# Kernel optimization log

Measured on AMD Instinct MI355X. Metric: run time of the kernel, lower is better.

Reference implementation:

```python
import jax, jax.numpy as jnp
import numpy as np

V = [8192, 2048, 512, 128, 32]   # vertex counts per mesh level
S = 9                            # spiral length
T = 64                           # number of audio frames
OC = [32, 64, 64, 128]           # out_channels
LAT = 64                         # latent_channels


def _spiral_conv(x, idx, w, b):
    # x: [B, Vi, C], idx: [Vi, S] -> gather spiral neighborhoods, flatten, linear
    B = x.shape[0]
    n, s = idx.shape
    g = x[:, idx.reshape(-1), :].reshape(B, n, -1)  # [B, Vi, S*C]
    return g @ w + b


def _pool(x, row, col, val, out_size):
    # sparse COO matmul along vertex dim: out[b, r, :] += val * x[b, c, :]
    g = x[:, col, :] * val[None, :, None]
    return jnp.zeros((x.shape[0], out_size, x.shape[2]), x.dtype).at[:, row, :].add(g)


def setup_inputs():
    key = jax.random.key(0)
    keys = iter(jax.random.split(key, 80))
    def nrm(shape, scale=0.05):
        return jax.random.normal(next(keys), shape, jnp.float32) * scale
    inp = {}
    inp["hidden_states"] = jax.random.normal(next(keys), (1, T, 768), jnp.float32)
    inp["actor"] = jax.random.normal(next(keys), (1, V[0], 3), jnp.float32)
    inp["audio_w"] = nrm((768, LAT)); inp["audio_b"] = jnp.zeros((LAT,), jnp.float32)
    enc_dims = [(3 * S, OC[0]), (OC[0] * S, OC[1]), (OC[1] * S, OC[2]), (OC[2] * S, OC[3])]
    for i, (a, b) in enumerate(enc_dims):
        inp[f"enc{i}_w"] = nrm((a, b)); inp[f"enc{i}_b"] = jnp.zeros((b,), jnp.float32)
    inp["enc_lat_w"] = nrm((V[4] * OC[3], LAT)); inp["enc_lat_b"] = jnp.zeros((LAT,), jnp.float32)
    inp["dec_lin_w"] = nrm((2 * LAT, V[4] * OC[3])); inp["dec_lin_b"] = jnp.zeros((V[4] * OC[3],), jnp.float32)
    dec_dims = [(OC[3] * S, OC[3]), (OC[3] * S, OC[2]), (OC[2] * S, OC[1]), (OC[1] * S, OC[0])]
    for i, (a, b) in enumerate(dec_dims):
        inp[f"dec{i}_w"] = nrm((a, b)); inp[f"dec{i}_b"] = jnp.zeros((b,), jnp.float32)
    inp["dec_out_w"] = nrm((OC[0] * S, 3)); inp["dec_out_b"] = jnp.zeros((3,), jnp.float32)
    for i in range(4):
        inp[f"spiral{i}"] = jax.random.randint(next(keys), (V[i], S), 0, V[i])
    for i in range(4):
        vin, vout = V[i], V[i + 1]
        inp[f"down{i}_row"] = jnp.repeat(jnp.arange(vout), 3)
        inp[f"down{i}_col"] = jax.random.randint(next(keys), (3 * vout,), 0, vin)
        inp[f"down{i}_val"] = jax.random.uniform(next(keys), (3 * vout,), jnp.float32) / 3.0
        inp[f"up{i}_row"] = jnp.repeat(jnp.arange(vin), 3)
        inp[f"up{i}_col"] = jax.random.randint(next(keys), (3 * vin,), 0, vout)
        inp[f"up{i}_val"] = jax.random.uniform(next(keys), (3 * vin,), jnp.float32) / 3.0
    return inp


def reference(hidden_states, actor, audio_w, audio_b,
              enc0_w, enc0_b, enc1_w, enc1_b, enc2_w, enc2_b, enc3_w, enc3_b,
              enc_lat_w, enc_lat_b,
              dec_lin_w, dec_lin_b, dec0_w, dec0_b, dec1_w, dec1_b,
              dec2_w, dec2_b, dec3_w, dec3_b, dec_out_w, dec_out_b,
              spiral0, spiral1, spiral2, spiral3,
              down0_row, down0_col, down0_val, down1_row, down1_col, down1_val,
              down2_row, down2_col, down2_val, down3_row, down3_col, down3_val,
              up0_row, up0_col, up0_val, up1_row, up1_col, up1_val,
              up2_row, up2_col, up2_val, up3_row, up3_col, up3_val):
    spirals = [spiral0, spiral1, spiral2, spiral3]
    enc_p = [(enc0_w, enc0_b), (enc1_w, enc1_b), (enc2_w, enc2_b), (enc3_w, enc3_b)]
    dec_p = [(dec0_w, dec0_b), (dec1_w, dec1_b), (dec2_w, dec2_b), (dec3_w, dec3_b)]
    down = [(down0_row, down0_col, down0_val), (down1_row, down1_col, down1_val),
            (down2_row, down2_col, down2_val), (down3_row, down3_col, down3_val)]
    up = [(up0_row, up0_col, up0_val), (up1_row, up1_col, up1_val),
          (up2_row, up2_col, up2_val), (up3_row, up3_col, up3_val)]

    # ---- encode(actor): conv -> elu -> pool per level, then flatten linear ----
    x = actor  # [1, V0, 3]
    for i in range(4):
        w, b = enc_p[i]
        x = jax.nn.elu(_spiral_conv(x, spirals[i], w, b))
        r, c, v = down[i]
        x = _pool(x, r, c, v, V[i + 1])
    actor_emb = x.reshape(1, -1) @ enc_lat_w + enc_lat_b  # [1, LAT]

    # ---- audio embedding and latent concat ----
    audio_emb = hidden_states[0] @ audio_w + audio_b       # [T, LAT]
    latent = jnp.concatenate(
        [audio_emb, jnp.broadcast_to(actor_emb, audio_emb.shape)], axis=-1)  # [T, 2*LAT]

    # ---- decode all frames at once (original loops per frame; batched over T) ----
    x = (latent @ dec_lin_w + dec_lin_b).reshape(-1, V[4], OC[3])  # [T, V4, OC3]
    for i in range(4):
        lvl = 3 - i
        r, c, v = up[lvl]
        x = _pool(x, r, c, v, V[lvl])
        w, b = dec_p[i]
        x = jax.nn.elu(_spiral_conv(x, spirals[lvl], w, b))
    x = _spiral_conv(x, spirals[0], dec_out_w, dec_out_b)  # [T, V0, 3]
    return x + actor  # broadcast actor (displacement prediction), pred_sequence[1:]
```

## Files before the change

### kernel.cpp

```cpp
#include <hip/hip_runtime.h>
#include <hip/hip_bf16.h>

typedef __hip_bfloat16 bf16;
typedef __attribute__((ext_vector_type(8))) short short8v;
typedef __attribute__((ext_vector_type(16))) float f32x16;

__device__ __forceinline__ float tof(float v){ return v; }
__device__ __forceinline__ float tof(bf16 v){ return __bfloat162float(v); }
__device__ __forceinline__ void sto(float* p, float v){ *p = v; }
__device__ __forceinline__ void sto(bf16* p, float v){ *p = __float2bfloat16(v); }
__device__ __forceinline__ short f2bs(float f){ bf16 h = __float2bfloat16(f); return *(short*)&h; }
__device__ __forceinline__ float bsu2f(short s){
    return __uint_as_float(((unsigned)(unsigned short)s) << 16);
}

__device__ __forceinline__ void sto4(float* p, float4 v){ *(float4*)p = v; }
__device__ __forceinline__ void sto4(bf16* p, float4 v){
    short4 s; s.x=f2bs(v.x); s.y=f2bs(v.y); s.z=f2bs(v.z); s.w=f2bs(v.w);
    *(short4*)p = s;
}

__device__ __forceinline__ void swz_t(int b, int bs, int& t, int& rem){
    int x = b & 7, k = b >> 3;
    t = x*8 + (k >> bs);
    rem = k & ((1 << bs) - 1);
}

__global__ __launch_bounds__(256) void k_prep(
    const float* __restrict__ w0, const float* __restrict__ w1,
    const float* __restrict__ w2, const float* __restrict__ w3,
    const float* __restrict__ w4,
    short* __restrict__ wt0, short* __restrict__ wt1,
    short* __restrict__ wt2, short* __restrict__ wt3,
    short* __restrict__ wt4,
    const float* __restrict__ hs, const float* __restrict__ aw,
    const float* __restrict__ ab, float* __restrict__ aemb)
{
    __shared__ float red[4][64];
    int b = blockIdx.x, tid = threadIdx.x;
    if (b < 1080){
        const float* w; short* wt; int K, nsh, i;
        if      (b < 576) { w = w0; wt = wt0; K = 1152; nsh = 7; i = b*256 + tid; }
        else if (b < 864) { w = w1; wt = wt1; K = 1152; nsh = 6; i = (b-576)*256 + tid; }
        else if (b < 1008){ w = w2; wt = wt2; K = 576;  nsh = 6; i = (b-864)*256 + tid; }
        else              { w = w3; wt = wt3; K = 576;  nsh = 5; i = (b-1008)*256 + tid; }
        int k = i >> nsh, n = i & ((1 << nsh) - 1);
        wt[n*K + k] = f2bs(w[i]);
    } else if (b < 1116){
        int i = (b - 1080)*256 + tid;
        int k = i >> 5, n = i & 31;
        wt4[n*288 + k] = (n < 3) ? f2bs(w4[k*3 + n]) : (short)0;
    } else {
        int t = b - 1116;
        int kg = tid >> 6, l = tid & 63;
        const float* h = hs + t*768;
        float acc = 0.f;
        int k0 = kg*192;
        #pragma unroll 8
        for (int k = k0; k < k0 + 192; k++) acc += h[k] * aw[k*64 + l];
        red[kg][l] = acc;
        __syncthreads();
        if (kg == 0)
            aemb[t*64 + l] = red[0][l] + red[1][l] + red[2][l] + red[3][l] + ab[l];
    }
}

__global__ __launch_bounds__(256) void k_enclat(const float* __restrict__ flat,
    const float* __restrict__ w, const float* __restrict__ b, float* __restrict__ out)
{
    __shared__ float red[256];
    int l = blockIdx.x, tid = threadIdx.x;
    float acc = 0.f;
    for (int k = tid; k < 4096; k += 256) acc += flat[k] * w[k*64 + l];
    red[tid] = acc; __syncthreads();
    for (int s = 128; s > 0; s >>= 1){ if (tid < s) red[tid] += red[tid+s]; __syncthreads(); }
    if (tid == 0) out[l] = red[0] + b[l];
}

__global__ __launch_bounds__(256) void k_declin4(const float* __restrict__ ae,
    const float* __restrict__ pe, const float* __restrict__ w, const float* __restrict__ b,
    bf16* __restrict__ out)
{
    int n4 = blockIdx.x*256 + threadIdx.x;
    int t = blockIdx.y;
    float4 acc = *(const float4*)&b[n4*4];
    const float* a = ae + t*64;
    #pragma unroll 4
    for (int k = 0; k < 64; k++){
        float av = a[k];
        float4 wv = *(const float4*)&w[(size_t)k*4096 + n4*4];
        acc.x += av*wv.x; acc.y += av*wv.y; acc.z += av*wv.z; acc.w += av*wv.w;
    }
    #pragma unroll 4
    for (int k = 0; k < 64; k++){
        float pv = pe[k];
        float4 wv = *(const float4*)&w[(size_t)(64+k)*4096 + n4*4];
        acc.x += pv*wv.x; acc.y += pv*wv.y; acc.z += pv*wv.z; acc.w += pv*wv.w;
    }
    sto4(&out[(size_t)t*4096 + n4*4], acc);
}

__global__ __launch_bounds__(256) void k_pool4(const float* __restrict__ xin,
    const int* __restrict__ col, const float* __restrict__ val, float* __restrict__ out,
    int total4, int c4mask, int cs, int vomask, int vos, int Vi)
{
    int i = blockIdx.x*256 + threadIdx.x;
    if (i >= total4) return;
    int c4 = i & c4mask;
    int rv = i >> cs;
    int r  = rv & vomask;
    int t  = rv >> vos;
    int C  = (c4mask + 1) << 2;
    const float* xt = xin + (size_t)t * Vi * C;
    int r3 = 3*r;
    int j0 = col[r3], j1 = col[r3+1], j2 = col[r3+2];
    float v0 = val[r3], v1 = val[r3+1], v2 = val[r3+2];
    int c = c4 << 2;
    float4 a = *(const float4*)&xt[(size_t)j0*C + c];
    float4 b = *(const float4*)&xt[(size_t)j1*C + c];
    float4 d = *(const float4*)&xt[(size_t)j2*C + c];
    float4 o;
    o.x = v0*a.x + v1*b.x + v2*d.x;
    o.y = v0*a.y + v1*b.y + v2*d.y;
    o.z = v0*a.z + v1*b.z + v2*d.z;
    o.w = v0*a.w + v1*b.w + v2*d.w;
    sto4(&out[(size_t)i << 2], o);
}

__global__ __launch_bounds__(256) void k_poolb(const bf16* __restrict__ xin,
    const int* __restrict__ col, const float* __restrict__ val, bf16* __restrict__ out,
    int c8mask, int cs, int vom, int vshin, int cshift, int bs, int ept8)
{
    int t, rem; swz_t(blockIdx.x, bs, t, rem);
    int il = rem*256 + threadIdx.x;
    int c8 = il & c8mask;
    int r  = (il >> cs) & vom;
    size_t i = (size_t)t * ept8 + il;
    const bf16* xt = xin + ((size_t)t << (vshin + cshift));
    int r3 = 3*r;
    int j0 = col[r3], j1 = col[r3+1], j2 = col[r3+2];
    float v0 = val[r3], v1 = val[r3+1], v2 = val[r3+2];
    int c = c8 << 3;
    short8v a = *(const short8v*)&xt[((size_t)j0 << cshift) + c];
    short8v b = *(const short8v*)&xt[((size_t)j1 << cshift) + c];
    short8v d = *(const short8v*)&xt[((size_t)j2 << cshift) + c];
    short8v o;
    #pragma unroll
    for (int q = 0; q < 8; q++)
        o[q] = f2bs(v0*bsu2f(a[q]) + v1*bsu2f(b[q]) + v2*bsu2f(d[q]));
    *(short8v*)&out[i << 3] = o;
}

template<int KTOT, int CSHIFT, int NTOT, typename TOUT>
__global__ __launch_bounds__(256) void k_conv_p3(
    const bf16* __restrict__ xin, const int* __restrict__ spiral,
    const short* __restrict__ wt, const float* __restrict__ bias, TOUT* __restrict__ out,
    int vshift, int bs, int nbshift)
{
    constexpr int NCH  = KTOT >> 6;
    constexpr int CSUB = CSHIFT - 6;
    __shared__ short lds_a[2*128*72];
    __shared__ short lds_b[2*32*72];
    const int tid = threadIdx.x;
    const int lane = tid & 63;
    const int wv = tid >> 6;
    const int col = lane & 31;
    const int half = lane >> 5;

    int t, rem; swz_t(blockIdx.x, bs, t, rem);
    const int nb = rem & ((1 << nbshift) - 1);
    const int vt = rem >> nbshift;
    const int mbase = vt*128;
    const size_t xslab = (size_t)t << (vshift + CSHIFT);

    const int am = tid >> 3;
    const int ak = (tid & 7) << 3;
    const int bn = tid >> 3;
    const int bk = (tid & 7) << 3;

    short8v pa[3][4];
    short8v pb[3];

    auto issue = [&](int ch, int st){
        int s = ch >> CSUB;
        int coff = ((ch & ((1 << CSUB) - 1)) << 6) + ak;
        #pragma unroll
        for (int u = 0; u < 4; u++){
            int j = spiral[(mbase + am + u*32)*9 + s];
            pa[st][u] = *(const short8v*)&xin[xslab + ((size_t)j << CSHIFT) + coff];
        }
        pb[st] = *(const short8v*)&wt[(size_t)(nb*32 + bn)*KTOT + (ch << 6) + bk];
    };
    auto commit = [&](int ch, int st){
        short* la = lds_a + (ch & 1)*(128*72);
        short* lb = lds_b + (ch & 1)*(32*72);
        #pragma unroll
        for (int u = 0; u < 4; u++)
            *(short8v*)&la[(am + u*32)*72 + ak] = pa[st][u];
        *(short8v*)&lb[bn*72 + bk] = pb[st];
    };

    f32x16 acc;
    {
        float bv = bias[nb*32 + col];
        #pragma unroll
        for (int r = 0; r < 16; r++) acc[r] = bv;
    }

    issue(0, 0);
    issue(1, 1);
    issue(2, 2);
    commit(0, 0);
    __syncthreads();
    #pragma unroll
    for (int ch = 0; ch < NCH; ch++){
        if (ch + 3 < NCH) issue(ch + 3, ch % 3);
        const short* la = lds_a + (ch & 1)*(128*72);
        const short* lb = lds_b + (ch & 1)*(32*72);
        #pragma unroll
        for (int ks = 0; ks < 4; ks++){
            short8v b = *(const short8v*)&lb[col*72 + ks*16 + half*8];
            short8v a = *(const short8v*)&la[(wv*32 + col)*72 + ks*16 + half*8];
            acc = __builtin_amdgcn_mfma_f32_32x32x16_bf16(a, b, acc, 0, 0, 0);
        }
        if (ch + 1 < NCH) commit(ch + 1, (ch + 1) % 3);
        __syncthreads();
    }
    size_t mb = ((size_t)t << vshift) + mbase + wv*32;
    #pragma unroll
    for (int r = 0; r < 16; r++){
        int row = (r & 3) + 8*(r >> 2) + 4*half;
        float vv = acc[r];
        vv = vv > 0.f ? vv : __expf(vv) - 1.f;
        sto(&out[(mb + row)*NTOT + nb*32 + col], vv);
    }
}

__global__ __launch_bounds__(256) void k_outmfma(
    const bf16* __restrict__ xin, const int* __restrict__ spiral,
    const short* __restrict__ wt, const float* __restrict__ bias,
    const float* __restrict__ actor, float* __restrict__ out)
{
    __shared__ short lds_a[256*36];
    __shared__ short lds_b[32*36];
    const int tid = threadIdx.x;
    const int lane = tid & 63;
    const int wv = tid >> 6;
    const int col = lane & 31;
    const int half = lane >> 5;

    int t, rem; swz_t(blockIdx.x, 5, t, rem);
    const int mbase = rem*256;
    const size_t xslab = (size_t)t << 18;

    short8v pa[4];
    short8v pb;
    const int am = tid >> 2;
    const int ak = (tid & 3) << 3;

    auto issue = [&](int s){
        #pragma unroll
        for (int u = 0; u < 4; u++){
            int j = spiral[(mbase + am + u*64)*9 + s];
            pa[u] = *(const short8v*)&xin[xslab + ((size_t)j << 5) + ak];
        }
        if (tid < 128)
            pb = *(const short8v*)&wt[am*288 + s*32 + ak];
    };
    auto commit = [&](){
        #pragma unroll
        for (int u = 0; u < 4; u++)
            *(short8v*)&lds_a[(am + u*64)*36 + ak] = pa[u];
        if (tid < 128)
            *(short8v*)&lds_b[am*36 + ak] = pb;
    };

    f32x16 acc[2];
    {
        float bv = (col < 3) ? bias[col] : 0.f;
        #pragma unroll
        for (int h = 0; h < 2; h++)
            #pragma unroll
            for (int r = 0; r < 16; r++) acc[h][r] = bv;
    }

    issue(0); commit(); __syncthreads();
    #pragma unroll
    for (int s = 0; s < 9; s++){
        if (s + 1 < 9) issue(s + 1);
        #pragma unroll
        for (int ks = 0; ks < 2; ks++){
            short8v b = *(short8v*)&lds_b[col*36 + ks*16 + half*8];
            #pragma unroll
            for (int h = 0; h < 2; h++){
                short8v a = *(short8v*)&lds_a[(h*128 + wv*32 + col)*36 + ks*16 + half*8];
                acc[h] = __builtin_amdgcn_mfma_f32_32x32x16_bf16(a, b, acc[h], 0, 0, 0);
            }
        }
        __syncthreads();
        if (s + 1 < 9){ commit(); __syncthreads(); }
    }
    if (col < 3){
        #pragma unroll
        for (int h = 0; h < 2; h++){
            int rowb = mbase + h*128 + wv*32;
            #pragma unroll
            for (int r = 0; r < 16; r++){
                int row = rowb + (r & 3) + 8*(r >> 2) + 4*half;
                out[(((size_t)t << 13) + row)*3 + col] = acc[h][r] + actor[row*3 + col];
            }
        }
    }
}

template<typename TIN>
__global__ __launch_bounds__(256) void k_conv(const TIN* __restrict__ xin,
    const int* __restrict__ spiral, const float* __restrict__ w, const float* __restrict__ bias,
    float* __restrict__ out, int TV, int V, int vshift, int C, int O2, int o2shift,
    int K, int KP, int MT)
{
    extern __shared__ float lds[];
    const int S = 9;
    int tid = threadIdx.x;
    int O = O2 << 1;
    int gmbase = blockIdx.x * MT;

    int total = MT * K;
    for (int e = tid; e < total; e += 256){
        int m = e / K, k = e - m*K;
        int gm = gmbase + m;
        if (gm < TV){
            int t = gm >> vshift, v = gm & (V-1);
            int s = k / C, c = k - s*C;
            int jj = spiral[v*S + s];
            lds[m*KP + k] = tof(xin[((size_t)t*V + jj)*C + c]);
        }
    }
    __syncthreads();

    int m = tid >> o2shift;
    int o = tid & (O2 - 1);
    int gm = gmbase + m;
    if (gm >= TV) return;
    const float* g  = lds + m*KP;
    const float* wp = w + 2*o;
    float acc0 = bias[2*o];
    float acc1 = bias[2*o+1];
    int K4 = K & ~3;
    for (int k = 0; k < K4; k += 4){
        float4 g4 = *(const float4*)(g + k);
        float2 w0 = *(const float2*)(wp + (size_t)k    *O);
        float2 w1 = *(const float2*)(wp + (size_t)(k+1)*O);
        float2 w2 = *(const float2*)(wp + (size_t)(k+2)*O);
        float2 w3 = *(const float2*)(wp + (size_t)(k+3)*O);
        acc0 += g4.x*w0.x + g4.y*w1.x + g4.z*w2.x + g4.w*w3.x;
        acc1 += g4.x*w0.y + g4.y*w1.y + g4.z*w2.y + g4.w*w3.y;
    }
    for (int k = K4; k < K; k++){
        float gv = g[k];
        acc0 += gv * wp[(size_t)k*O];
        acc1 += gv * wp[(size_t)k*O + 1];
    }
    acc0 = acc0 > 0.f ? acc0 : __expf(acc0) - 1.f;
    acc1 = acc1 > 0.f ? acc1 : __expf(acc1) - 1.f;
    float2 r; r.x = acc0; r.y = acc1;
    *(float2*)(out + (size_t)gm*O + 2*o) = r;
}

extern "C" void kernel_launch(void* const* d_in, const int* in_sizes, int n_in,
                              void* d_out, int out_size, void* d_ws, size_t ws_size,
                              hipStream_t stream)
{
    (void)n_in; (void)out_size; (void)ws_size;
    const float* hs        = (const float*)d_in[0];
    const float* actor     = (const float*)d_in[1];
    const float* audio_w   = (const float*)d_in[2];
    const float* audio_b   = (const float*)d_in[3];
    const float* enc_w[4]  = {(const float*)d_in[4],(const float*)d_in[6],(const float*)d_in[8],(const float*)d_in[10]};
    const float* enc_b[4]  = {(const float*)d_in[5],(const float*)d_in[7],(const float*)d_in[9],(const float*)d_in[11]};
    const float* enc_lat_w = (const float*)d_in[12];
    const float* enc_lat_b = (const float*)d_in[13];
    const float* dec_lin_w = (const float*)d_in[14];
    const float* dec_lin_b = (const float*)d_in[15];
    const float* dec_w[4]  = {(const float*)d_in[16],(const float*)d_in[18],(const float*)d_in[20],(const float*)d_in[22]};
    const float* dec_b[4]  = {(const float*)d_in[17],(const float*)d_in[19],(const float*)d_in[21],(const float*)d_in[23]};
    const float* dec_out_w = (const float*)d_in[24];
    const float* dec_out_b = (const float*)d_in[25];
    const int*   spiral[4] = {(const int*)d_in[26],(const int*)d_in[27],(const int*)d_in[28],(const int*)d_in[29]};

    const int* dcol[4]; const float* dval[4]; const int* ucol[4]; const float* uval[4];
    bool interleaved = (in_sizes[33] == 3*8192);
    for (int i = 0; i < 4; i++){
        if (interleaved){
            int b = 30 + 6*i;
            dcol[i] = (const int*)d_in[b+1]; dval[i] = (const float*)d_in[b+2];
            ucol[i] = (const int*)d_in[b+4]; uval[i] = (const float*)d_in[b+5];
        } else {
            dcol[i] = (const int*)d_in[31+3*i]; dval[i] = (const float*)d_in[32+3*i];
            ucol[i] = (const int*)d_in[43+3*i]; uval[i] = (const float*)d_in[44+3*i];
        }
    }

    char* ws = (char*)d_ws;
    size_t off = 0;
    auto alloc = [&](size_t bytes)->char* {
        char* p = ws + off; off += (bytes + 255) & ~(size_t)255; return p;
    };
    float* encX0 = (float*)alloc((size_t)262144*4);
    float* encP0 = (float*)alloc((size_t)65536*4);
    float* encX1 = (float*)alloc((size_t)131072*4);
    float* encP1 = (float*)alloc((size_t)32768*4);
    float* encX2 = (float*)alloc((size_t)32768*4);
    float* encP2 = (float*)alloc((size_t)8192*4);
    float* encX3 = (float*)alloc((size_t)16384*4);
    float* encP3 = (float*)alloc((size_t)4096*4);
    float* aemb  = (float*)alloc((size_t)4096*4);
    float* pemb  = (float*)alloc((size_t)64*4);
    short* wt0   = (short*)alloc((size_t)147456*2);
    short* wt1   = (short*)alloc((size_t)73728*2);
    short* wt2   = (short*)alloc((size_t)36864*2);
    short* wt3   = (short*)alloc((size_t)18432*2);
    short* wt4   = (short*)alloc((size_t)9216*2);
    bf16*  Pb    = (bf16*)alloc((size_t)36*1048576);
    bf16*  Qb    = (bf16*)alloc((size_t)68*1048576);

    k_prep<<<1180,256,0,stream>>>(dec_w[0], dec_w[1], dec_w[2], dec_w[3], dec_out_w,
                                  wt0, wt1, wt2, wt3, wt4, hs, audio_w, audio_b, aemb);

    k_conv<float><<<512,256, 16*28*4, stream>>>(actor, spiral[0], enc_w[0], enc_b[0], encX0, 8192, 8192,13,   3,16,4,  27,  28,16);
    k_pool4<<<64,256,0,stream>>>(encX0, dcol[0], dval[0], encP0, 16384, 7,3, 2047,11, 8192);
    k_conv<float><<<256,256, 8*292*4, stream>>>(encP0, spiral[1], enc_w[1], enc_b[1], encX1, 2048, 2048,11,  32,32,5, 288, 292, 8);
    k_pool4<<<32,256,0,stream>>>(encX1, dcol[1], dval[1], encP1, 8192, 15,4, 511,9, 2048);
    k_conv<float><<<64,256, 8*580*4, stream>>>(encP1, spiral[2], enc_w[2], enc_b[2], encX2, 512, 512,9,  64,32,5, 576, 580, 8);
    k_pool4<<<8,256,0,stream>>>(encX2, dcol[2], dval[2], encP2, 2048, 15,4, 127,7, 512);
    k_conv<float><<<32,256, 4*580*4, stream>>>(encP2, spiral[3], enc_w[3], enc_b[3], encX3, 128, 128,7,  64,64,6, 576, 580, 4);
    k_pool4<<<4,256,0,stream>>>(encX3, dcol[3], dval[3], encP3, 1024, 31,5, 31,5, 128);
    k_enclat<<<64,256,0,stream>>>(encP3, enc_lat_w, enc_lat_b, pemb);

    k_declin4<<<dim3(4,64),256,0,stream>>>(aemb, pemb, dec_lin_w, dec_lin_b, Pb);

    k_poolb<<<512,256,0,stream>>>(Pb, ucol[3], uval[3], Qb, 15,4, 127, 5,7, 3, 2048);
    k_conv_p3<1152,7,128,bf16><<<256,256,0,stream>>>(Qb, spiral[3], wt0, dec_b[0], Pb, 7, 2, 2);

    k_poolb<<<2048,256,0,stream>>>(Pb, ucol[2], uval[2], Qb, 15,4, 511, 7,7, 5, 8192);
    k_conv_p3<1152,7,64,bf16><<<512,256,0,stream>>>(Qb, spiral[2], wt1, dec_b[1], Pb, 9, 3, 1);

    k_poolb<<<4096,256,0,stream>>>(Pb, ucol[1], uval[1], Qb, 7,3, 2047, 9,6, 6, 16384);
    k_conv_p3<576,6,64,bf16><<<2048,256,0,stream>>>(Qb, spiral[1], wt2, dec_b[2], Pb, 11, 5, 1);

    k_poolb<<<16384,256,0,stream>>>(Pb, ucol[0], uval[0], Qb, 7,3, 8191, 11,6, 8, 65536);
    k_conv_p3<576,6,32,bf16><<<4096,256,0,stream>>>(Qb, spiral[0], wt3, dec_b[3], Pb, 13, 6, 0);

    k_outmfma<<<2048,256,0,stream>>>(Pb, spiral[0], wt4, dec_out_b, actor, (float*)d_out);
}
```

Baseline: 436.4 us.

## Load spiral-gathered A fragments directly into MFMA registers in output conv

The final output spiral conv no longer stages gathered neighbour rows through LDS with per-step barriers. Each lane now loads its A fragment straight from global memory using spiral indices held in registers. The whole weight matrix is preloaded into LDS once, and each block covers 128 rows instead of 256, which doubles the grid. This drops the barrier-heavy staging loop, but the 16-byte gathers go directly to registers with no explicit prefetching and the weight tile is reloaded by twice as many blocks.

```diff
diff --git a/kernel.cpp b/kernel.cpp
--- a/kernel.cpp
+++ b/kernel.cpp
@@ -236,79 +236,54 @@
     }
 }
 
-__global__ __launch_bounds__(256) void k_outmfma(
+__global__ __launch_bounds__(256) void k_outdg(
     const bf16* __restrict__ xin, const int* __restrict__ spiral,
     const short* __restrict__ wt, const float* __restrict__ bias,
     const float* __restrict__ actor, float* __restrict__ out)
 {
-    __shared__ short lds_a[256*36];
-    __shared__ short lds_b[32*36];
+    __shared__ short lds_b[32*292];
     const int tid = threadIdx.x;
     const int lane = tid & 63;
     const int wv = tid >> 6;
     const int col = lane & 31;
     const int half = lane >> 5;
 
-    int t, rem; swz_t(blockIdx.x, 5, t, rem);
-    const int mbase = rem*256;
+    int t, rem; swz_t(blockIdx.x, 6, t, rem);
+    const int rowb = rem*128 + wv*32;
+    const int vrow = rowb + col;
     const size_t xslab = (size_t)t << 18;
 
-    short8v pa[4];
-    short8v pb;
-    const int am = tid >> 2;
-    const int ak = (tid & 3) << 3;
-
-    auto issue = [&](int s){
-        #pragma unroll
-        for (int u = 0; u < 4; u++){
-            int j = spiral[(mbase + am + u*64)*9 + s];
-            pa[u] = *(const short8v*)&xin[xslab + ((size_t)j << 5) + ak];
-        }
-        if (tid < 128)
-            pb = *(const short8v*)&wt[am*288 + s*32 + ak];
-    };
-    auto commit = [&](){
-        #pragma unroll
-        for (int u = 0; u < 4; u++)
-            *(short8v*)&lds_a[(am + u*64)*36 + ak] = pa[u];
-        if (tid < 128)
-            *(short8v*)&lds_b[am*36 + ak] = pb;
-    };
-
-    f32x16 acc[2];
+    int j[9];
+    #pragma unroll
+    for (int s = 0; s < 9; s++) j[s] = spiral[vrow*9 + s];
+
+    for (int e = tid; e < 1152; e += 256){
+        int n = e / 36, kk = (e - n*36) << 3;
+        *(short8v*)&lds_b[n*292 + kk] = *(const short8v*)&wt[n*288 + kk];
+    }
+    __syncthreads();
+
+    f32x16 acc;
     {
         float bv = (col < 3) ? bias[col] : 0.f;
         #pragma unroll
-        for (int h = 0; h < 2; h++)
-            #pragma unroll
-            for (int r = 0; r < 16; r++) acc[h][r] = bv;
-    }
-
-    issue(0); commit(); __syncthreads();
+        for (int r = 0; r < 16; r++) acc[r] = bv;
+    }
+
     #pragma unroll
-    for (int s = 0; s < 9; s++){
-        if (s + 1 < 9) issue(s + 1);
-        #pragma unroll
-        for (int ks = 0; ks < 2; ks++){
-            short8v b = *(short8v*)&lds_b[col*36 + ks*16 + half*8];
-            #pragma unroll
-            for (int h = 0; h < 2; h++){
-                short8v a = *(short8v*)&lds_a[(h*128 + wv*32 + col)*36 + ks*16 + half*8];
-                acc[h] = __builtin_amdgcn_mfma_f32_32x32x16_bf16(a, b, acc[h], 0, 0, 0);
-            }
-        }
-        __syncthreads();
-        if (s + 1 < 9){ commit(); __syncthreads(); }
-    }
+    for (int ls = 0; ls < 18; ls++){
+        int s = ls >> 1;
+        int c = ((ls & 1) << 4) + half*8;
+        short8v a = *(const short8v*)&xin[xslab + ((size_t)j[s] << 5) + c];
+        short8v b = *(short8v*)&lds_b[col*292 + ls*16 + half*8];
+        acc = __builtin_amdgcn_mfma_f32_32x32x16_bf16(a, b, acc, 0, 0, 0);
+    }
+
     if (col < 3){
         #pragma unroll
-        for (int h = 0; h < 2; h++){
-            int rowb = mbase + h*128 + wv*32;
-            #pragma unroll
-            for (int r = 0; r < 16; r++){
-                int row = rowb + (r & 3) + 8*(r >> 2) + 4*half;
-                out[(((size_t)t << 13) + row)*3 + col] = acc[h][r] + actor[row*3 + col];
-            }
+        for (int r = 0; r < 16; r++){
+            int row = rowb + (r & 3) + 8*(r >> 2) + 4*half;
+            out[(((size_t)t << 13) + row)*3 + col] = acc[r] + actor[row*3 + col];
         }
     }
 }
@@ -451,5 +426,5 @@
     k_poolb<<<16384,256,0,stream>>>(Pb, ucol[0], uval[0], Qb, 7,3, 8191, 11,6, 8, 65536);
     k_conv_p3<576,6,32,bf16><<<4096,256,0,stream>>>(Qb, spiral[0], wt3, dec_b[3], Pb, 13, 6, 0);
 
-    k_outmfma<<<2048,256,0,stream>>>(Pb, spiral[0], wt4, dec_out_b, actor, (float*)d_out);
-}
+    k_outdg<<<4096,256,0,stream>>>(Pb, spiral[0], wt4, dec_out_b, actor, (float*)d_out);
+}
```

Measured after the change: 441.7 us. About the same (+1.2%).

## Fuse encoder conv/pool chain into one cooperative kernel with grid syncs

Applied to the files above, without the earlier changes.

Replaces the nine separate encoder launches (four spiral convs, four pools, latent linear) with a single cooperative kernel of 256 blocks. Grid-wide syncs sit between stages, and each stage uses grid-stride loops. This removes launch overhead and inter-kernel gaps for the small encoder stages. The cost is grid-sync latency and fixed parallelism: the first conv stage now loops over tiles with 256 blocks instead of 512.

```diff
diff --git a/kernel.cpp b/kernel.cpp
--- a/kernel.cpp
+++ b/kernel.cpp
@@ -1,5 +1,8 @@
 #include <hip/hip_runtime.h>
 #include <hip/hip_bf16.h>
+#include <hip/hip_cooperative_groups.h>
+
+namespace cg = cooperative_groups;
 
 typedef __hip_bfloat16 bf16;
 typedef __attribute__((ext_vector_type(8))) short short8v;
@@ -65,16 +68,123 @@
     }
 }
 
-__global__ __launch_bounds__(256) void k_enclat(const float* __restrict__ flat,
-    const float* __restrict__ w, const float* __restrict__ b, float* __restrict__ out)
-{
-    __shared__ float red[256];
-    int l = blockIdx.x, tid = threadIdx.x;
-    float acc = 0.f;
-    for (int k = tid; k < 4096; k += 256) acc += flat[k] * w[k*64 + l];
-    red[tid] = acc; __syncthreads();
-    for (int s = 128; s > 0; s >>= 1){ if (tid < s) red[tid] += red[tid+s]; __syncthreads(); }
-    if (tid == 0) out[l] = red[0] + b[l];
+struct EncArgs {
+    const float* actor;
+    const int* sp[4];
+    const float* w[4];
+    const float* b[4];
+    const int* dc[4];
+    const float* dv[4];
+    const float* elw; const float* elb;
+    float* X0; float* P0; float* X1; float* P1;
+    float* X2; float* P2; float* X3; float* P3;
+    float* pemb;
+};
+
+__device__ __forceinline__ void conv_stage(const float* __restrict__ xin,
+    const int* __restrict__ spiral, const float* __restrict__ w, const float* __restrict__ bias,
+    float* __restrict__ out, int TV, int C, int O2, int o2shift, int K, int KP, int MT,
+    float* lds)
+{
+    int tid = threadIdx.x;
+    int O = O2 << 1;
+    for (int gmbase = blockIdx.x*MT; gmbase < TV; gmbase += gridDim.x*MT){
+        int total = MT*K;
+        for (int e = tid; e < total; e += 256){
+            int m = e / K, k = e - m*K;
+            int gm = gmbase + m;
+            if (gm < TV){
+                int s = k / C, c = k - s*C;
+                int jj = spiral[gm*9 + s];
+                lds[m*KP + k] = xin[(size_t)jj*C + c];
+            }
+        }
+        __syncthreads();
+        int m = tid >> o2shift;
+        int o = tid & (O2 - 1);
+        int gm = gmbase + m;
+        if (gm < TV){
+            const float* gr = lds + m*KP;
+            const float* wp = w + 2*o;
+            float acc0 = bias[2*o];
+            float acc1 = bias[2*o+1];
+            int K4 = K & ~3;
+            for (int k = 0; k < K4; k += 4){
+                float4 g4 = *(const float4*)(gr + k);
+                float2 w0 = *(const float2*)(wp + (size_t)k    *O);
+                float2 w1 = *(const float2*)(wp + (size_t)(k+1)*O);
+                float2 w2 = *(const float2*)(wp + (size_t)(k+2)*O);
+                float2 w3 = *(const float2*)(wp + (size_t)(k+3)*O);
+                acc0 += g4.x*w0.x + g4.y*w1.x + g4.z*w2.x + g4.w*w3.x;
+                acc1 += g4.x*w0.y + g4.y*w1.y + g4.z*w2.y + g4.w*w3.y;
+            }
+            for (int k = K4; k < K; k++){
+                float gv = gr[k];
+                acc0 += gv * wp[(size_t)k*O];
+                acc1 += gv * wp[(size_t)k*O + 1];
+            }
+            acc0 = acc0 > 0.f ? acc0 : __expf(acc0) - 1.f;
+            acc1 = acc1 > 0.f ? acc1 : __expf(acc1) - 1.f;
+            float2 r; r.x = acc0; r.y = acc1;
+            *(float2*)(out + (size_t)gm*O + 2*o) = r;
+        }
+        __syncthreads();
+    }
+}
+
+__device__ __forceinline__ void pool_stage(const float* __restrict__ xin,
+    const int* __restrict__ col, const float* __restrict__ val, float* __restrict__ out,
+    int total4, int c4mask, int cs, int vomask)
+{
+    int C = (c4mask + 1) << 2;
+    for (int i = blockIdx.x*256 + threadIdx.x; i < total4; i += gridDim.x*256){
+        int c4 = i & c4mask;
+        int r  = (i >> cs) & vomask;
+        int r3 = 3*r;
+        int j0 = col[r3], j1 = col[r3+1], j2 = col[r3+2];
+        float v0 = val[r3], v1 = val[r3+1], v2 = val[r3+2];
+        int c = c4 << 2;
+        float4 a = *(const float4*)&xin[(size_t)j0*C + c];
+        float4 b = *(const float4*)&xin[(size_t)j1*C + c];
+        float4 d = *(const float4*)&xin[(size_t)j2*C + c];
+        float4 o;
+        o.x = v0*a.x + v1*b.x + v2*d.x;
+        o.y = v0*a.y + v1*b.y + v2*d.y;
+        o.z = v0*a.z + v1*b.z + v2*d.z;
+        o.w = v0*a.w + v1*b.w + v2*d.w;
+        sto4(&out[(size_t)i << 2], o);
+    }
+}
+
+__global__ __launch_bounds__(256) void k_encmega(EncArgs a)
+{
+    cg::grid_group g = cg::this_grid();
+    __shared__ float lds[4672];
+
+    conv_stage(a.actor, a.sp[0], a.w[0], a.b[0], a.X0, 8192,  3, 16,4,  27, 28,16, lds);
+    g.sync();
+    pool_stage(a.X0, a.dc[0], a.dv[0], a.P0, 16384, 7,3, 2047);
+    g.sync();
+    conv_stage(a.P0, a.sp[1], a.w[1], a.b[1], a.X1, 2048, 32, 32,5, 288,292, 8, lds);
+    g.sync();
+    pool_stage(a.X1, a.dc[1], a.dv[1], a.P1, 8192, 15,4, 511);
+    g.sync();
+    conv_stage(a.P1, a.sp[2], a.w[2], a.b[2], a.X2, 512,  64, 32,5, 576,580, 8, lds);
+    g.sync();
+    pool_stage(a.X2, a.dc[2], a.dv[2], a.P2, 2048, 15,4, 127);
+    g.sync();
+    conv_stage(a.P2, a.sp[3], a.w[3], a.b[3], a.X3, 128,  64, 64,6, 576,580, 4, lds);
+    g.sync();
+    pool_stage(a.X3, a.dc[3], a.dv[3], a.P3, 1024, 31,5, 31);
+    g.sync();
+    if (blockIdx.x < 64){
+        int l = blockIdx.x, tid = threadIdx.x;
+        float acc = 0.f;
+        for (int k = tid; k < 4096; k += 256) acc += a.P3[k] * a.elw[k*64 + l];
+        lds[tid] = acc; __syncthreads();
+        for (int s = 128; s > 0; s >>= 1){ if (tid < s) lds[tid] += lds[tid+s]; __syncthreads(); }
+        if (tid == 0) a.pemb[l] = lds[0] + a.elb[l];
+    }
 }
 
 __global__ __launch_bounds__(256) void k_declin4(const float* __restrict__ ae,
@@ -98,33 +208,6 @@
         acc.x += pv*wv.x; acc.y += pv*wv.y; acc.z += pv*wv.z; acc.w += pv*wv.w;
     }
     sto4(&out[(size_t)t*4096 + n4*4], acc);
-}
-
-__global__ __launch_bounds__(256) void k_pool4(const float* __restrict__ xin,
-    const int* __restrict__ col, const float* __restrict__ val, float* __restrict__ out,
-    int total4, int c4mask, int cs, int vomask, int vos, int Vi)
-{
-    int i = blockIdx.x*256 + threadIdx.x;
-    if (i >= total4) return;
-    int c4 = i & c4mask;
-    int rv = i >> cs;
-    int r  = rv & vomask;
-    int t  = rv >> vos;
-    int C  = (c4mask + 1) << 2;
-    const float* xt = xin + (size_t)t * Vi * C;
-    int r3 = 3*r;
-    int j0 = col[r3], j1 = col[r3+1], j2 = col[r3+2];
-    float v0 = val[r3], v1 = val[r3+1], v2 = val[r3+2];
-    int c = c4 << 2;
-    float4 a = *(const float4*)&xt[(size_t)j0*C + c];
-    float4 b = *(const float4*)&xt[(size_t)j1*C + c];
-    float4 d = *(const float4*)&xt[(size_t)j2*C + c];
-    float4 o;
-    o.x = v0*a.x + v1*b.x + v2*d.x;
-    o.y = v0*a.y + v1*b.y + v2*d.y;
-    o.z = v0*a.z + v1*b.z + v2*d.z;
-    o.w = v0*a.w + v1*b.w + v2*d.w;
-    sto4(&out[(size_t)i << 2], o);
 }
 
 __global__ __launch_bounds__(256) void k_poolb(const bf16* __restrict__ xin,
@@ -311,60 +394,6 @@
             }
         }
     }
-}
-
-template<typename TIN>
-__global__ __launch_bounds__(256) void k_conv(const TIN* __restrict__ xin,
-    const int* __restrict__ spiral, const float* __restrict__ w, const float* __restrict__ bias,
-    float* __restrict__ out, int TV, int V, int vshift, int C, int O2, int o2shift,
-    int K, int KP, int MT)
-{
-    extern __shared__ float lds[];
-    const int S = 9;
-    int tid = threadIdx.x;
-    int O = O2 << 1;
-    int gmbase = blockIdx.x * MT;
-
-    int total = MT * K;
-    for (int e = tid; e < total; e += 256){
-        int m = e / K, k = e - m*K;
-        int gm = gmbase + m;
-        if (gm < TV){
-            int t = gm >> vshift, v = gm & (V-1);
-            int s = k / C, c = k - s*C;
-            int jj = spiral[v*S + s];
-            lds[m*KP + k] = tof(xin[((size_t)t*V + jj)*C + c]);
-        }
-    }
-    __syncthreads();
-
-    int m = tid >> o2shift;
-    int o = tid & (O2 - 1);
-    int gm = gmbase + m;
-    if (gm >= TV) return;
-    const float* g  = lds + m*KP;
-    const float* wp = w + 2*o;
-    float acc0 = bias[2*o];
-    float acc1 = bias[2*o+1];
-    int K4 = K & ~3;
-    for (int k = 0; k < K4; k += 4){
-        float4 g4 = *(const float4*)(g + k);
-        float2 w0 = *(const float2*)(wp + (size_t)k    *O);
-        float2 w1 = *(const float2*)(wp + (size_t)(k+1)*O);
-        float2 w2 = *(const float2*)(wp + (size_t)(k+2)*O);
-        float2 w3 = *(const float2*)(wp + (size_t)(k+3)*O);
-        acc0 += g4.x*w0.x + g4.y*w1.x + g4.z*w2.x + g4.w*w3.x;
-        acc1 += g4.x*w0.y + g4.y*w1.y + g4.z*w2.y + g4.w*w3.y;
-    }
-    for (int k = K4; k < K; k++){
-        float gv = g[k];
-        acc0 += gv * wp[(size_t)k*O];
-        acc1 += gv * wp[(size_t)k*O + 1];
-    }
-    acc0 = acc0 > 0.f ? acc0 : __expf(acc0) - 1.f;
-    acc1 = acc1 > 0.f ? acc1 : __expf(acc1) - 1.f;
-    float2 r; r.x = acc0; r.y = acc1;
-    *(float2*)(out + (size_t)gm*O + 2*o) = r;
 }
 
 extern "C" void kernel_launch(void* const* d_in, const int* in_sizes, int n_in,
@@ -427,15 +456,22 @@
     k_prep<<<1180,256,0,stream>>>(dec_w[0], dec_w[1], dec_w[2], dec_w[3], dec_out_w,
                                   wt0, wt1, wt2, wt3, wt4, hs, audio_w, audio_b, aemb);
 
-    k_conv<float><<<512,256, 16*28*4, stream>>>(actor, spiral[0], enc_w[0], enc_b[0], encX0, 8192, 8192,13,   3,16,4,  27,  28,16);
-    k_pool4<<<64,256,0,stream>>>(encX0, dcol[0], dval[0], encP0, 16384, 7,3, 2047,11, 8192);
-    k_conv<float><<<256,256, 8*292*4, stream>>>(encP0, spiral[1], enc_w[1], enc_b[1], encX1, 2048, 2048,11,  32,32,5, 288, 292, 8);
-    k_pool4<<<32,256,0,stream>>>(encX1, dcol[1], dval[1], encP1, 8192, 15,4, 511,9, 2048);
-    k_conv<float><<<64,256, 8*580*4, stream>>>(encP1, spiral[2], enc_w[2], enc_b[2], encX2, 512, 512,9,  64,32,5, 576, 580, 8);
-    k_pool4<<<8,256,0,stream>>>(encX2, dcol[2], dval[2], encP2, 2048, 15,4, 127,7, 512);
-    k_conv<float><<<32,256, 4*580*4, stream>>>(encP2, spiral[3], enc_w[3], enc_b[3], encX3, 128, 128,7,  64,64,6, 576, 580, 4);
-    k_pool4<<<4,256,0,stream>>>(encX3, dcol[3], dval[3], encP3, 1024, 31,5, 31,5, 128);
-    k_enclat<<<64,256,0,stream>>>(encP3, enc_lat_w, enc_lat_b, pemb);
+    EncArgs ea;
+    ea.actor = actor;
+    for (int i = 0; i < 4; i++){
+        ea.sp[i] = spiral[i];
+        ea.w[i]  = enc_w[i];
+        ea.b[i]  = enc_b[i];
+        ea.dc[i] = dcol[i];
+        ea.dv[i] = dval[i];
+    }
+    ea.elw = enc_lat_w; ea.elb = enc_lat_b;
+    ea.X0 = encX0; ea.P0 = encP0; ea.X1 = encX1; ea.P1 = encP1;
+    ea.X2 = encX2; ea.P2 = encP2; ea.X3 = encX3; ea.P3 = encP3;
+    ea.pemb = pemb;
+    void* eparams[] = { &ea };
+    hipLaunchCooperativeKernel((const void*)k_encmega, dim3(256), dim3(256),
+                               eparams, 0, stream);
 
     k_declin4<<<dim3(4,64),256,0,stream>>>(aemb, pemb, dec_lin_w, dec_lin_b, Pb);
 
```

After: 691.6 us. 58.5% more time.
